# Kernel tuning notes

Hardware: AMD Instinct MI355X
Metric: run time of the kernel (lower is better)

Reference implementation:

```python
import jax, jax.numpy as jnp
import numpy as np

N = 4096
CIN = 128
COUT = 128
J = 2
SLOPE = 0.2        # LeakyReLU negative slope (GAT-style)
NEG = -9.0e15      # mask fill value from the source
ATT = J * COUT     # att_slice


def _leaky(v):
    return jnp.where(v >= 0, v, SLOPE * v)


def setup_inputs() -> dict:
    key = jax.random.key(0)
    ks = jax.random.split(key, 12)
    x = jax.random.normal(ks[0], (N, CIN), dtype=jnp.float32)

    def sparse_op(k):
        kv, km = jax.random.split(k)
        vals = jax.random.normal(kv, (N, N), dtype=jnp.float32)
        mask = jax.random.uniform(km, (N, N)) < 0.05
        return jnp.where(mask, vals, 0.0)

    Lu = sparse_op(ks[1])
    Ld = sparse_op(ks[2])
    P = jax.random.normal(ks[3], (N, N), dtype=jnp.float32) * 0.01  # harmonic projector

    s = 1.0 / np.sqrt(CIN)
    Wi_w = jax.random.uniform(ks[4], (J, CIN, COUT), minval=-s, maxval=s)
    Wi_b = jax.random.uniform(ks[5], (J, COUT), minval=-s, maxval=s)
    Ws_w = jax.random.uniform(ks[6], (J, CIN, COUT), minval=-s, maxval=s)
    Ws_b = jax.random.uniform(ks[7], (J, COUT), minval=-s, maxval=s)
    Wh_w = jax.random.uniform(ks[8], (CIN, COUT), minval=-s, maxval=s)
    Wh_b = jax.random.uniform(ks[9], (COUT,), minval=-s, maxval=s)
    att_irr = jax.random.normal(ks[10], (2 * ATT, 1), dtype=jnp.float32) * 0.1
    att_sol = jax.random.normal(ks[11], (2 * ATT, 1), dtype=jnp.float32) * 0.1
    return {"x": x, "Lu": Lu, "Ld": Ld, "P": P,
            "Wi_w": Wi_w, "Wi_b": Wi_b, "Ws_w": Ws_w, "Ws_b": Ws_b,
            "Wh_w": Wh_w, "Wh_b": Wh_b, "att_irr": att_irr, "att_sol": att_sol}


def reference(x, Lu, Ld, P, Wi_w, Wi_b, Ws_w, Ws_b, Wh_w, Wh_b, att_irr, att_sol):
    n = x.shape[0]
    # concat_j W_irr[j](x) -> [N, J*COUT] (j-major matches torch.cat along dim=1)
    x_irr = (jnp.einsum('nc,jco->njo', x, Wi_w) + Wi_b[None]).reshape(n, ATT)
    x_sol = (jnp.einsum('nc,jco->njo', x, Ws_w) + Ws_b[None]).reshape(n, ATT)

    # GAT-style scores: E[i,j] = leaky(s1[i] + s2[j])
    E_irr = _leaky(x_irr @ att_irr[:ATT] + (x_irr @ att_irr[ATT:]).T)
    E_sol = _leaky(x_sol @ att_sol[:ATT] + (x_sol @ att_sol[ATT:]).T)
    E_irr = jnp.where(Ld != 0, E_irr, NEG)
    E_sol = jnp.where(Lu != 0, E_sol, NEG)
    alpha_irr = jax.nn.softmax(E_irr, axis=1)  # dropout: eval mode -> identity
    alpha_sol = jax.nn.softmax(E_sol, axis=1)

    z = (alpha_irr @ x) @ Wi_w[0] + Wi_b[0] + (alpha_sol @ x) @ Ws_w[0] + Ws_b[0]
    for p in range(1, J):  # Laplacian-power aggregation
        alpha_irr = alpha_irr @ Ld
        alpha_sol = alpha_sol @ Lu
        z = z + (alpha_irr @ x) @ Wi_w[p] + Wi_b[p]
        z = z + (alpha_sol @ x) @ Ws_w[p] + Ws_b[p]
    z = z + (P @ x) @ Wh_w + Wh_b
    return z
```

## Files before the change

kernel.cpp:

```cpp
#include <hip/hip_runtime.h>

#define NN 4096
#define IDX_CAP 512
#define SEG_CAP 160
#define SLOPE 0.2f

typedef float f4_t __attribute__((ext_vector_type(4)));

#define V_OFF     0
#define C_OFF     512
#define BT_OFF    516
#define S_OFF     1024
#define HXI_OFF   32768
#define HXS_OFF   (HXI_OFF + NN*128)
#define UI_OFF    (HXS_OFF + NN*128)
#define US_OFF    (UI_OFF + NN*128)
#define XWH_OFF   (US_OFF + NN*128)
#define OI_OFF    (XWH_OFF + NN*128)
#define OS_OFF    (OI_OFF + NN*128)
#define ZP_OFF    (OS_OFF + NN*128)
#define WS_FLOATS (ZP_OFF + 8*NN*128)
#define IDX_BYTE_OFF ((size_t)WS_FLOATS * 4)
#define CNT_BYTE_OFF (IDX_BYTE_OFF + (size_t)2*NN*IDX_CAP*2)

__global__ __launch_bounds__(128) void k_prep(
    const float* __restrict__ Wi_w, const float* __restrict__ Wi_b,
    const float* __restrict__ Ws_w, const float* __restrict__ Ws_b,
    const float* __restrict__ Wh_b, const float* __restrict__ att_irr,
    const float* __restrict__ att_sol, float* __restrict__ ws) {
  const int t = threadIdx.x;
  float v1i = 0.f, v2i = 0.f, v1s = 0.f, v2s = 0.f;
  for (int j = 0; j < 2; ++j) {
    for (int o = 0; o < 128; ++o) {
      const float wi = Wi_w[j*16384 + t*128 + o];
      const float wv = Ws_w[j*16384 + t*128 + o];
      v1i += wi * att_irr[j*128 + o];
      v2i += wi * att_irr[256 + j*128 + o];
      v1s += wv * att_sol[j*128 + o];
      v2s += wv * att_sol[256 + j*128 + o];
    }
  }
  ws[V_OFF + t]       = v1i;
  ws[V_OFF + 128 + t] = v2i;
  ws[V_OFF + 256 + t] = v1s;
  ws[V_OFF + 384 + t] = v2s;
  ws[BT_OFF + t] = Wi_b[t] + Wi_b[128 + t] + Ws_b[t] + Ws_b[128 + t] + Wh_b[t];
  if (t < 4) {
    const float* bb = (t < 2) ? Wi_b : Ws_b;
    const float* aa = ((t < 2) ? att_irr : att_sol) + ((t & 1) ? 256 : 0);
    float c = 0.f;
    for (int k = 0; k < 256; ++k) c += bb[k] * aa[k];
    ws[C_OFF + t] = c;
  }
}

__global__ __launch_bounds__(256) void k_scores(const float* __restrict__ x,
                                                float* __restrict__ ws) {
  const int wave = threadIdx.x >> 6, lane = threadIdx.x & 63;
  const int row = blockIdx.x * 4 + wave;
  const float* v = ws + V_OFF;
  const float x0 = x[row*128 + lane];
  const float x1 = x[row*128 + 64 + lane];
  float p0 = x0 * v[lane]       + x1 * v[64 + lane];
  float p1 = x0 * v[128 + lane] + x1 * v[192 + lane];
  float p2 = x0 * v[256 + lane] + x1 * v[320 + lane];
  float p3 = x0 * v[384 + lane] + x1 * v[448 + lane];
  #pragma unroll
  for (int off = 32; off; off >>= 1) {
    p0 += __shfl_down(p0, off);
    p1 += __shfl_down(p1, off);
    p2 += __shfl_down(p2, off);
    p3 += __shfl_down(p3, off);
  }
  if (lane == 0) {
    ws[S_OFF + row]          = p0 + ws[C_OFF + 0];
    ws[S_OFF + NN + row]     = p1 + ws[C_OFF + 1];
    ws[S_OFF + 2*NN + row]   = p2 + ws[C_OFF + 2];
    ws[S_OFF + 3*NN + row]   = p3 + ws[C_OFF + 3];
  }
}

__global__ __launch_bounds__(256) void k_spmm_emit(
    const float* __restrict__ Ld, const float* __restrict__ Lu,
    const float* __restrict__ x, float* __restrict__ ws,
    unsigned short* __restrict__ idxbuf, int* __restrict__ cntbuf) {
  const int row = blockIdx.x & (NN - 1);
  const int br  = blockIdx.x >> 12;
  const float* __restrict__ Lrow = (br ? Lu : Ld) + (size_t)row * NN;
  float* __restrict__ Hx = ws + (br ? HXS_OFF : HXI_OFF);
  unsigned short* __restrict__ idxg = idxbuf + (size_t)(br*NN + row) * IDX_CAP;
  const float2* __restrict__ x2 = (const float2*)x;
  const int t = threadIdx.x;
  const int w = t >> 6, lane = t & 63;
  const unsigned long long lmask = (1ull << lane) - 1ull;

  __shared__ short jseg[4][SEG_CAP];
  __shared__ float vseg[4][SEG_CAP];
  __shared__ int   wcnt[4];
  __shared__ int   off[5];
  __shared__ short jl[IDX_CAP];
  __shared__ float vl[IDX_CAP];
  __shared__ float red[4][128];

  const f4_t* __restrict__ Lrow4 = (const f4_t*)Lrow;
  f4_t lv[4];
  #pragma unroll
  for (int i = 0; i < 4; ++i) lv[i] = __builtin_nontemporal_load(&Lrow4[i*256 + t]);

  int base = 0;
  #pragma unroll
  for (int i = 0; i < 4; ++i) {
    #pragma unroll
    for (int c = 0; c < 4; ++c) {
      const float v = lv[i][c];
      const unsigned long long bm = __ballot(v != 0.f);
      if (v != 0.f) {
        const int pos = base + (int)__popcll(bm & lmask);
        if (pos < SEG_CAP) {
          jseg[w][pos] = (short)((i*256 + t)*4 + c);
          vseg[w][pos] = v;
        }
      }
      base += (int)__popcll(bm);
    }
  }
  if (lane == 0) wcnt[w] = base;
  __syncthreads();
  if (t == 0) {
    int o = 0, ov = 0;
    #pragma unroll
    for (int s = 0; s < 4; ++s) { off[s] = o; ov |= (wcnt[s] > SEG_CAP); o += wcnt[s]; }
    off[4] = (ov || o > IDX_CAP) ? (IDX_CAP + 1) : o;
    cntbuf[br*NN + row] = off[4];
  }
  __syncthreads();
  const int m = off[4];

  if (m <= IDX_CAP) {
    const int o = off[w], c = wcnt[w];
    for (int k = lane; k < c; k += 64) {
      const short j = jseg[w][k];
      jl[o + k] = j;
      vl[o + k] = vseg[w][k];
      idxg[o + k] = (unsigned short)j;
    }
  }
  __syncthreads();

  float acc0 = 0.f, acc1 = 0.f;
  if (m <= IDX_CAP) {
    int p = w;
    for (; p + 28 < m; p += 32) {
      const int j0 = jl[p],    j1 = jl[p+4],  j2 = jl[p+8],  j3 = jl[p+12];
      const int j4 = jl[p+16], j5 = jl[p+20], j6 = jl[p+24], j7 = jl[p+28];
      const float v0 = vl[p],    v1 = vl[p+4],  v2 = vl[p+8],  v3 = vl[p+12];
      const float v4 = vl[p+16], v5 = vl[p+20], v6 = vl[p+24], v7 = vl[p+28];
      const float2 g0 = x2[j0*64 + lane];
      const float2 g1 = x2[j1*64 + lane];
      const float2 g2 = x2[j2*64 + lane];
      const float2 g3 = x2[j3*64 + lane];
      const float2 g4 = x2[j4*64 + lane];
      const float2 g5 = x2[j5*64 + lane];
      const float2 g6 = x2[j6*64 + lane];
      const float2 g7 = x2[j7*64 + lane];
      acc0 += v0*g0.x; acc1 += v0*g0.y;
      acc0 += v1*g1.x; acc1 += v1*g1.y;
      acc0 += v2*g2.x; acc1 += v2*g2.y;
      acc0 += v3*g3.x; acc1 += v3*g3.y;
      acc0 += v4*g4.x; acc1 += v4*g4.y;
      acc0 += v5*g5.x; acc1 += v5*g5.y;
      acc0 += v6*g6.x; acc1 += v6*g6.y;
      acc0 += v7*g7.x; acc1 += v7*g7.y;
    }
    for (; p < m; p += 4) {
      const int j = jl[p]; const float v = vl[p];
      const float2 g = x2[j*64 + lane];
      acc0 += v*g.x; acc1 += v*g.y;
    }
  } else {
    for (int j = w*1024; j < (w+1)*1024; ++j) {
      const float v = Lrow[j];
      if (v != 0.f) {
        const float2 g = x2[j*64 + lane];
        acc0 += v*g.x; acc1 += v*g.y;
      }
    }
  }
  red[w][lane*2]     = acc0;
  red[w][lane*2 + 1] = acc1;
  __syncthreads();
  if (t < 128)
    Hx[row*128 + t] = red[0][t] + red[1][t] + red[2][t] + red[3][t];
}

__global__ __launch_bounds__(256) void k_ugemm(
    const float* __restrict__ x, const float* __restrict__ Wi_w,
    const float* __restrict__ Ws_w, const float* __restrict__ Wh_w,
    float* __restrict__ ws) {
  const int rb = blockIdx.x;
  const int sel = blockIdx.y;
  const float* A[2]; const float* W[2]; int npass; float* out;
  if (sel == 0)      { A[0]=x; W[0]=Wi_w; A[1]=ws+HXI_OFF; W[1]=Wi_w+16384; npass=2; out=ws+UI_OFF; }
  else if (sel == 1) { A[0]=x; W[0]=Ws_w; A[1]=ws+HXS_OFF; W[1]=Ws_w+16384; npass=2; out=ws+US_OFF; }
  else               { A[0]=x; W[0]=Wh_w; A[1]=nullptr;    W[1]=nullptr;    npass=1; out=ws+XWH_OFF; }

  __shared__ __align__(16) float At[32][33];
  __shared__ __align__(16) float Wt[32][132];
  const int t = threadIdx.x;
  const int rg = t >> 4, cg = t & 15;
  const int r0 = rb * 32;
  float acc[2][8];
  #pragma unroll
  for (int i = 0; i < 2; ++i)
    #pragma unroll
    for (int j = 0; j < 8; ++j) acc[i][j] = 0.f;

  for (int ps = 0; ps < npass; ++ps) {
    const float* __restrict__ Ap = A[ps];
    const float* __restrict__ Wp = W[ps];
    for (int k0 = 0; k0 < 128; k0 += 32) {
      __syncthreads();
      {
        const int row = t >> 3, kq = t & 7;
        const float4 av = *(const float4*)&Ap[(r0 + row)*128 + k0 + kq*4];
        At[row][kq*4+0] = av.x; At[row][kq*4+1] = av.y;
        At[row][kq*4+2] = av.z; At[row][kq*4+3] = av.w;
      }
      #pragma unroll
      for (int l = 0; l < 4; ++l) {
        const int idx = t + l*256;
        const int kr = idx >> 5, c4 = idx & 31;
        const float4 wv = *(const float4*)&Wp[(k0 + kr)*128 + c4*4];
        Wt[kr][c4*4+0] = wv.x; Wt[kr][c4*4+1] = wv.y;
        Wt[kr][c4*4+2] = wv.z; Wt[kr][c4*4+3] = wv.w;
      }
      __syncthreads();
      #pragma unroll
      for (int k = 0; k < 32; ++k) {
        const float a0 = At[rg*2 + 0][k];
        const float a1 = At[rg*2 + 1][k];
        const float4 b0 = *(const float4*)&Wt[k][cg*8];
        const float4 b1 = *(const float4*)&Wt[k][cg*8 + 4];
        acc[0][0] += a0*b0.x; acc[0][1] += a0*b0.y; acc[0][2] += a0*b0.z; acc[0][3] += a0*b0.w;
        acc[0][4] += a0*b1.x; acc[0][5] += a0*b1.y; acc[0][6] += a0*b1.z; acc[0][7] += a0*b1.w;
        acc[1][0] += a1*b0.x; acc[1][1] += a1*b0.y; acc[1][2] += a1*b0.z; acc[1][3] += a1*b0.w;
        acc[1][4] += a1*b1.x; acc[1][5] += a1*b1.y; acc[1][6] += a1*b1.z; acc[1][7] += a1*b1.w;
      }
    }
  }
  #pragma unroll
  for (int i = 0; i < 2; ++i) {
    const int r = r0 + rg*2 + i;
    #pragma unroll
    for (int j = 0; j < 8; ++j) out[r*128 + cg*8 + j] = acc[i][j];
  }
}

__global__ __launch_bounds__(256) void k_pgemm(const float* __restrict__ P,
                                               const float* __restrict__ ws,
                                               float* __restrict__ zpart) {
  const int rbl = blockIdx.x;
  const int kz  = blockIdx.y;
  const float* __restrict__ Xw = ws + XWH_OFF;

  __shared__ __align__(16) float Pt[64][33];
  __shared__ __align__(16) float Xt[32][132];
  const int t = threadIdx.x;
  const int rg = t >> 4, cg = t & 15;
  const int r0 = rbl * 64;
  const int kbase = kz * 512;
  float acc[4][8];
  #pragma unroll
  for (int i = 0; i < 4; ++i)
    #pragma unroll
    for (int j = 0; j < 8; ++j) acc[i][j] = 0.f;

  for (int k0 = kbase; k0 < kbase + 512; k0 += 32) {
    __syncthreads();
    #pragma unroll
    for (int l = 0; l < 2; ++l) {
      const int idx = t + l*256;
      const int row = idx >> 3, kq = idx & 7;
      const float4 pv = *(const float4*)&P[(size_t)(r0 + row)*NN + k0 + kq*4];
      Pt[row][kq*4+0] = pv.x; Pt[row][kq*4+1] = pv.y;
      Pt[row][kq*4+2] = pv.z; Pt[row][kq*4+3] = pv.w;
    }
    #pragma unroll
    for (int l = 0; l < 4; ++l) {
      const int idx = t + l*256;
      const int kr = idx >> 5, c4 = idx & 31;
      const float4 xv = *(const float4*)&Xw[(k0 + kr)*128 + c4*4];
      Xt[kr][c4*4+0] = xv.x; Xt[kr][c4*4+1] = xv.y;
      Xt[kr][c4*4+2] = xv.z; Xt[kr][c4*4+3] = xv.w;
    }
    __syncthreads();
    #pragma unroll
    for (int k = 0; k < 32; ++k) {
      const float a0 = Pt[rg*4 + 0][k];
      const float a1 = Pt[rg*4 + 1][k];
      const float a2 = Pt[rg*4 + 2][k];
      const float a3 = Pt[rg*4 + 3][k];
      const float4 b0 = *(const float4*)&Xt[k][cg*8];
      const float4 b1 = *(const float4*)&Xt[k][cg*8 + 4];
      acc[0][0] += a0*b0.x; acc[0][1] += a0*b0.y; acc[0][2] += a0*b0.z; acc[0][3] += a0*b0.w;
      acc[0][4] += a0*b1.x; acc[0][5] += a0*b1.y; acc[0][6] += a0*b1.z; acc[0][7] += a0*b1.w;
      acc[1][0] += a1*b0.x; acc[1][1] += a1*b0.y; acc[1][2] += a1*b0.z; acc[1][3] += a1*b0.w;
      acc[1][4] += a1*b1.x; acc[1][5] += a1*b1.y; acc[1][6] += a1*b1.z; acc[1][7] += a1*b1.w;
      acc[2][0] += a2*b0.x; acc[2][1] += a2*b0.y; acc[2][2] += a2*b0.z; acc[2][3] += a2*b0.w;
      acc[2][4] += a2*b1.x; acc[2][5] += a2*b1.y; acc[2][6] += a2*b1.z; acc[2][7] += a2*b1.w;
      acc[3][0] += a3*b0.x; acc[3][1] += a3*b0.y; acc[3][2] += a3*b0.z; acc[3][3] += a3*b0.w;
      acc[3][4] += a3*b1.x; acc[3][5] += a3*b1.y; acc[3][6] += a3*b1.z; acc[3][7] += a3*b1.w;
    }
  }
  float* __restrict__ zp = zpart + (size_t)kz * NN * 128;
  #pragma unroll
  for (int i = 0; i < 4; ++i) {
    const int r = r0 + rg*4 + i;
    #pragma unroll
    for (int j = 0; j < 8; ++j) zp[r*128 + cg*8 + j] = acc[i][j];
  }
}

__global__ __launch_bounds__(256) void k_attn(
    const float* __restrict__ Ld, const float* __restrict__ Lu,
    float* __restrict__ ws, const unsigned short* __restrict__ idxbuf,
    const int* __restrict__ cntbuf) {
  const int row = blockIdx.x & (NN - 1);
  const int br  = blockIdx.x >> 12;
  const float* __restrict__ U = ws + (br ? US_OFF : UI_OFF);
  const float2* __restrict__ U2 = (const float2*)U;
  float* __restrict__ O = ws + (br ? OS_OFF : OI_OFF);
  const float s1 = ws[S_OFF + (br ? 2*NN : 0) + row];
  const float* __restrict__ s2a = ws + S_OFF + (br ? 3*NN : NN);
  const int cnt = cntbuf[br*NN + row];
  const int t = threadIdx.x;
  const int w = t >> 6, lane = t & 63;

  __shared__ int   jl[IDX_CAP];
  __shared__ float el[IDX_CAP];
  __shared__ float red[4][128];
  __shared__ float rsum[256];
  __shared__ float dsh[4];

  float acc0 = 0.f, acc1 = 0.f;
  if (cnt > 0 && cnt <= IDX_CAP) {
    const unsigned short* __restrict__ idx = idxbuf + (size_t)(br*NN + row) * IDX_CAP;
    float dpart = 0.f;
    for (int p = t; p < cnt; p += 256) {
      const int j = idx[p];
      const float sc = s1 + s2a[j];
      const float e = expf(sc >= 0.f ? sc : SLOPE * sc);
      jl[p] = j; el[p] = e; dpart += e;
    }
    rsum[t] = dpart;
    __syncthreads();
    if (t < 128) rsum[t] += rsum[t + 128];
    __syncthreads();
    if (t < 64) {
      float v = rsum[t] + rsum[t + 64];
      #pragma unroll
      for (int off = 32; off; off >>= 1) v += __shfl_down(v, off);
      if (t == 0) dsh[0] = v;
    }
    __syncthreads();
    const float den = dsh[0];
    int p = w;
    for (; p + 28 < cnt; p += 32) {
      const int j0 = jl[p],    j1 = jl[p+4],  j2 = jl[p+8],  j3 = jl[p+12];
      const int j4 = jl[p+16], j5 = jl[p+20], j6 = jl[p+24], j7 = jl[p+28];
      const float e0 = el[p],    e1 = el[p+4],  e2 = el[p+8],  e3 = el[p+12];
      const float e4 = el[p+16], e5 = el[p+20], e6 = el[p+24], e7 = el[p+28];
      const float2 g0 = U2[j0*64 + lane];
      const float2 g1 = U2[j1*64 + lane];
      const float2 g2 = U2[j2*64 + lane];
      const float2 g3 = U2[j3*64 + lane];
      const float2 g4 = U2[j4*64 + lane];
      const float2 g5 = U2[j5*64 + lane];
      const float2 g6 = U2[j6*64 + lane];
      const float2 g7 = U2[j7*64 + lane];
      acc0 += e0*g0.x; acc1 += e0*g0.y;
      acc0 += e1*g1.x; acc1 += e1*g1.y;
      acc0 += e2*g2.x; acc1 += e2*g2.y;
      acc0 += e3*g3.x; acc1 += e3*g3.y;
      acc0 += e4*g4.x; acc1 += e4*g4.y;
      acc0 += e5*g5.x; acc1 += e5*g5.y;
      acc0 += e6*g6.x; acc1 += e6*g6.y;
      acc0 += e7*g7.x; acc1 += e7*g7.y;
    }
    for (; p < cnt; p += 4) {
      const int j = jl[p]; const float e = el[p];
      const float2 g = U2[j*64 + lane];
      acc0 += e*g.x; acc1 += e*g.y;
    }
    red[w][lane*2]     = acc0;
    red[w][lane*2 + 1] = acc1;
    __syncthreads();
    if (t < 128)
      O[row*128 + t] = (red[0][t] + red[1][t] + red[2][t] + red[3][t]) / den;
  } else if (cnt == 0) {
    for (int j = w*1024; j < (w+1)*1024; ++j) {
      const float2 g = U2[j*64 + lane];
      acc0 += g.x; acc1 += g.y;
    }
    red[w][lane*2]     = acc0;
    red[w][lane*2 + 1] = acc1;
    __syncthreads();
    if (t < 128)
      O[row*128 + t] = (red[0][t] + red[1][t] + red[2][t] + red[3][t]) * (1.f / NN);
  } else {
    const float* __restrict__ Lrow = (br ? Lu : Ld) + (size_t)row * NN;
    float dp = 0.f;
    for (int j = w*1024; j < (w+1)*1024; ++j) {
      const float v = Lrow[j];
      if (v != 0.f) {
        const float sc = s1 + s2a[j];
        const float e = expf(sc >= 0.f ? sc : SLOPE * sc);
        const float2 g = U2[j*64 + lane];
        acc0 += e*g.x; acc1 += e*g.y;
        dp += e;
      }
    }
    if (lane == 0) dsh[w] = dp;
    red[w][lane*2]     = acc0;
    red[w][lane*2 + 1] = acc1;
    __syncthreads();
    const float den = dsh[0] + dsh[1] + dsh[2] + dsh[3];
    if (t < 128)
      O[row*128 + t] = (red[0][t] + red[1][t] + red[2][t] + red[3][t]) / den;
  }
}

__global__ __launch_bounds__(256) void k_combine(const float* __restrict__ ws,
                                                 float* __restrict__ z) {
  const int i = blockIdx.x * 256 + threadIdx.x;
  const int col = i & 127;
  float acc = ws[BT_OFF + col] + ws[OI_OFF + i] + ws[OS_OFF + i];
  #pragma unroll
  for (int kz = 0; kz < 8; ++kz) acc += ws[ZP_OFF + kz*NN*128 + i];
  z[i] = acc;
}

extern "C" void kernel_launch(void* const* d_in, const int* in_sizes, int n_in,
                              void* d_out, int out_size, void* d_ws, size_t ws_size,
                              hipStream_t stream) {
  const float* x       = (const float*)d_in[0];
  const float* Lu      = (const float*)d_in[1];
  const float* Ld      = (const float*)d_in[2];
  const float* P       = (const float*)d_in[3];
  const float* Wi_w    = (const float*)d_in[4];
  const float* Wi_b    = (const float*)d_in[5];
  const float* Ws_w    = (const float*)d_in[6];
  const float* Ws_b    = (const float*)d_in[7];
  const float* Wh_w    = (const float*)d_in[8];
  const float* Wh_b    = (const float*)d_in[9];
  const float* att_irr = (const float*)d_in[10];
  const float* att_sol = (const float*)d_in[11];
  float* z  = (float*)d_out;
  float* ws = (float*)d_ws;
  unsigned short* idxbuf = (unsigned short*)((char*)d_ws + IDX_BYTE_OFF);
  int*            cntbuf = (int*)((char*)d_ws + CNT_BYTE_OFF);

  k_prep<<<1, 128, 0, stream>>>(Wi_w, Wi_b, Ws_w, Ws_b, Wh_b, att_irr, att_sol, ws);
  k_scores<<<1024, 256, 0, stream>>>(x, ws);
  k_spmm_emit<<<2 * NN, 256, 0, stream>>>(Ld, Lu, x, ws, idxbuf, cntbuf);
  {
    dim3 g(128, 3);
    k_ugemm<<<g, 256, 0, stream>>>(x, Wi_w, Ws_w, Wh_w, ws);
  }
  {
    dim3 g(64, 8);
    k_pgemm<<<g, 256, 0, stream>>>(P, ws, ws + ZP_OFF);
  }
  k_attn<<<2 * NN, 256, 0, stream>>>(Ld, Lu, ws, idxbuf, cntbuf);
  k_combine<<<NN * 128 / 256, 256, 0, stream>>>(ws, z);
}
```

Before: 399.0 us.

## Co-schedule dense P GEMM with sparse SpMM and attention kernels via block-split fusion

Moves the x@Wh GEMM into a merged pre-kernel alongside the score computation. The dense P@(xWh) GEMM is split into two halves of the K range, and each half is fused into the same launch as the memory-bound sparse SpMM or attention kernel using a shared-memory union and block-index dispatch. The aim is to overlap compute-heavy GEMM blocks with gather-heavy sparse blocks and cut launch count. It also pads the Xt shared tile with an XI swizzle to reduce bank conflicts. The cost is larger per-block shared memory from the union, which can lower occupancy for the sparse blocks.

```diff
diff --git a/kernel.cpp b/kernel.cpp
--- a/kernel.cpp
+++ b/kernel.cpp
@@ -23,6 +23,20 @@
 #define IDX_BYTE_OFF ((size_t)WS_FLOATS * 4)
 #define CNT_BYTE_OFF (IDX_BYTE_OFF + (size_t)2*NN*IDX_CAP*2)
 
+#define XI(c) ((c) + (((c) >> 5) << 2))
+
+struct SmemGemm { float Pt[64][33]; float Xt[32][140]; };
+struct SmemSpmm {
+  short jseg[4][SEG_CAP]; float vseg[4][SEG_CAP];
+  int wcnt[4]; int off[5];
+  short jl[IDX_CAP]; float vl[IDX_CAP]; float red[4][128];
+};
+struct SmemAttn {
+  int jl[IDX_CAP]; float el[IDX_CAP]; float red[4][128];
+  float rsum[256]; float dsh[4];
+};
+union SmemU { SmemGemm g; SmemSpmm s; SmemAttn a; };
+
 __global__ __launch_bounds__(128) void k_prep(
     const float* __restrict__ Wi_w, const float* __restrict__ Wi_b,
     const float* __restrict__ Ws_w, const float* __restrict__ Ws_b,
@@ -54,38 +68,149 @@
   }
 }
 
-__global__ __launch_bounds__(256) void k_scores(const float* __restrict__ x,
-                                                float* __restrict__ ws) {
-  const int wave = threadIdx.x >> 6, lane = threadIdx.x & 63;
-  const int row = blockIdx.x * 4 + wave;
-  const float* v = ws + V_OFF;
-  const float x0 = x[row*128 + lane];
-  const float x1 = x[row*128 + 64 + lane];
-  float p0 = x0 * v[lane]       + x1 * v[64 + lane];
-  float p1 = x0 * v[128 + lane] + x1 * v[192 + lane];
-  float p2 = x0 * v[256 + lane] + x1 * v[320 + lane];
-  float p3 = x0 * v[384 + lane] + x1 * v[448 + lane];
-  #pragma unroll
-  for (int off = 32; off; off >>= 1) {
-    p0 += __shfl_down(p0, off);
-    p1 += __shfl_down(p1, off);
-    p2 += __shfl_down(p2, off);
-    p3 += __shfl_down(p3, off);
-  }
-  if (lane == 0) {
-    ws[S_OFF + row]          = p0 + ws[C_OFF + 0];
-    ws[S_OFF + NN + row]     = p1 + ws[C_OFF + 1];
-    ws[S_OFF + 2*NN + row]   = p2 + ws[C_OFF + 2];
-    ws[S_OFF + 3*NN + row]   = p3 + ws[C_OFF + 3];
-  }
-}
-
-__global__ __launch_bounds__(256) void k_spmm_emit(
+__global__ __launch_bounds__(256) void k_pre2(
+    const float* __restrict__ x, const float* __restrict__ Wh_w,
+    float* __restrict__ ws) {
+  __shared__ __align__(16) float At[32][33];
+  __shared__ __align__(16) float Wt[32][132];
+  const int t = threadIdx.x;
+
+  if (blockIdx.x < 128) {
+    const int rb = blockIdx.x;
+    float* out = ws + XWH_OFF;
+    const int rg = t >> 4, cg = t & 15;
+    const int r0 = rb * 32;
+    float acc[2][8];
+    #pragma unroll
+    for (int i = 0; i < 2; ++i)
+      #pragma unroll
+      for (int j = 0; j < 8; ++j) acc[i][j] = 0.f;
+    for (int k0 = 0; k0 < 128; k0 += 32) {
+      __syncthreads();
+      {
+        const int row = t >> 3, kq = t & 7;
+        const float4 av = *(const float4*)&x[(r0 + row)*128 + k0 + kq*4];
+        At[row][kq*4+0] = av.x; At[row][kq*4+1] = av.y;
+        At[row][kq*4+2] = av.z; At[row][kq*4+3] = av.w;
+      }
+      #pragma unroll
+      for (int l = 0; l < 4; ++l) {
+        const int idx = t + l*256;
+        const int kr = idx >> 5, c4 = idx & 31;
+        const float4 wv = *(const float4*)&Wh_w[(k0 + kr)*128 + c4*4];
+        Wt[kr][c4*4+0] = wv.x; Wt[kr][c4*4+1] = wv.y;
+        Wt[kr][c4*4+2] = wv.z; Wt[kr][c4*4+3] = wv.w;
+      }
+      __syncthreads();
+      #pragma unroll
+      for (int k = 0; k < 32; ++k) {
+        const float a0 = At[rg*2 + 0][k];
+        const float a1 = At[rg*2 + 1][k];
+        const float4 b0 = *(const float4*)&Wt[k][cg*8];
+        const float4 b1 = *(const float4*)&Wt[k][cg*8 + 4];
+        acc[0][0] += a0*b0.x; acc[0][1] += a0*b0.y; acc[0][2] += a0*b0.z; acc[0][3] += a0*b0.w;
+        acc[0][4] += a0*b1.x; acc[0][5] += a0*b1.y; acc[0][6] += a0*b1.z; acc[0][7] += a0*b1.w;
+        acc[1][0] += a1*b0.x; acc[1][1] += a1*b0.y; acc[1][2] += a1*b0.z; acc[1][3] += a1*b0.w;
+        acc[1][4] += a1*b1.x; acc[1][5] += a1*b1.y; acc[1][6] += a1*b1.z; acc[1][7] += a1*b1.w;
+      }
+    }
+    #pragma unroll
+    for (int i = 0; i < 2; ++i) {
+      const int r = r0 + rg*2 + i;
+      #pragma unroll
+      for (int j = 0; j < 8; ++j) out[r*128 + cg*8 + j] = acc[i][j];
+    }
+  } else {
+    const int wave = t >> 6, lane = t & 63;
+    const int row = (blockIdx.x - 128) * 4 + wave;
+    const float* v = ws + V_OFF;
+    const float x0 = x[row*128 + lane];
+    const float x1 = x[row*128 + 64 + lane];
+    float p0 = x0 * v[lane]       + x1 * v[64 + lane];
+    float p1 = x0 * v[128 + lane] + x1 * v[192 + lane];
+    float p2 = x0 * v[256 + lane] + x1 * v[320 + lane];
+    float p3 = x0 * v[384 + lane] + x1 * v[448 + lane];
+    #pragma unroll
+    for (int off = 32; off; off >>= 1) {
+      p0 += __shfl_down(p0, off);
+      p1 += __shfl_down(p1, off);
+      p2 += __shfl_down(p2, off);
+      p3 += __shfl_down(p3, off);
+    }
+    if (lane == 0) {
+      ws[S_OFF + row]          = p0 + ws[C_OFF + 0];
+      ws[S_OFF + NN + row]     = p1 + ws[C_OFF + 1];
+      ws[S_OFF + 2*NN + row]   = p2 + ws[C_OFF + 2];
+      ws[S_OFF + 3*NN + row]   = p3 + ws[C_OFF + 3];
+    }
+  }
+}
+
+__device__ __forceinline__ void pgemm_body(
+    const float* __restrict__ P, const float* __restrict__ Xw,
+    float* __restrict__ zpart, SmemU& sm, const int rbl, const int kz) {
+  const int t = threadIdx.x;
+  const int rg = t >> 4, cg = t & 15;
+  const int r0 = rbl * 64;
+  const int kbase = kz * 512;
+  float acc[4][8];
+  #pragma unroll
+  for (int i = 0; i < 4; ++i)
+    #pragma unroll
+    for (int j = 0; j < 8; ++j) acc[i][j] = 0.f;
+
+  for (int k0 = kbase; k0 < kbase + 512; k0 += 32) {
+    __syncthreads();
+    #pragma unroll
+    for (int l = 0; l < 2; ++l) {
+      const int idx = t + l*256;
+      const int row = idx >> 3, kq = idx & 7;
+      const float4 pv = *(const float4*)&P[(size_t)(r0 + row)*NN + k0 + kq*4];
+      sm.g.Pt[row][kq*4+0] = pv.x; sm.g.Pt[row][kq*4+1] = pv.y;
+      sm.g.Pt[row][kq*4+2] = pv.z; sm.g.Pt[row][kq*4+3] = pv.w;
+    }
+    #pragma unroll
+    for (int l = 0; l < 4; ++l) {
+      const int idx = t + l*256;
+      const int kr = idx >> 5, c4 = idx & 31;
+      const float4 xv = *(const float4*)&Xw[(k0 + kr)*128 + c4*4];
+      *(float4*)&sm.g.Xt[kr][XI(c4*4)] = xv;
+    }
+    __syncthreads();
+    #pragma unroll
+    for (int k = 0; k < 32; ++k) {
+      const float a0 = sm.g.Pt[rg*4 + 0][k];
+      const float a1 = sm.g.Pt[rg*4 + 1][k];
+      const float a2 = sm.g.Pt[rg*4 + 2][k];
+      const float a3 = sm.g.Pt[rg*4 + 3][k];
+      const float4 b0 = *(const float4*)&sm.g.Xt[k][XI(cg*8)];
+      const float4 b1 = *(const float4*)&sm.g.Xt[k][XI(cg*8 + 4)];
+      acc[0][0] += a0*b0.x; acc[0][1] += a0*b0.y; acc[0][2] += a0*b0.z; acc[0][3] += a0*b0.w;
+      acc[0][4] += a0*b1.x; acc[0][5] += a0*b1.y; acc[0][6] += a0*b1.z; acc[0][7] += a0*b1.w;
+      acc[1][0] += a1*b0.x; acc[1][1] += a1*b0.y; acc[1][2] += a1*b0.z; acc[1][3] += a1*b0.w;
+      acc[1][4] += a1*b1.x; acc[1][5] += a1*b1.y; acc[1][6] += a1*b1.z; acc[1][7] += a1*b1.w;
+      acc[2][0] += a2*b0.x; acc[2][1] += a2*b0.y; acc[2][2] += a2*b0.z; acc[2][3] += a2*b0.w;
+      acc[2][4] += a2*b1.x; acc[2][5] += a2*b1.y; acc[2][6] += a2*b1.z; acc[2][7] += a2*b1.w;
+      acc[3][0] += a3*b0.x; acc[3][1] += a3*b0.y; acc[3][2] += a3*b0.z; acc[3][3] += a3*b0.w;
+      acc[3][4] += a3*b1.x; acc[3][5] += a3*b1.y; acc[3][6] += a3*b1.z; acc[3][7] += a3*b1.w;
+    }
+  }
+  float* __restrict__ zp = zpart + (size_t)kz * NN * 128;
+  #pragma unroll
+  for (int i = 0; i < 4; ++i) {
+    const int r = r0 + rg*4 + i;
+    #pragma unroll
+    for (int j = 0; j < 8; ++j) zp[r*128 + cg*8 + j] = acc[i][j];
+  }
+}
+
+__device__ __forceinline__ void spmm_body(
     const float* __restrict__ Ld, const float* __restrict__ Lu,
     const float* __restrict__ x, float* __restrict__ ws,
-    unsigned short* __restrict__ idxbuf, int* __restrict__ cntbuf) {
-  const int row = blockIdx.x & (NN - 1);
-  const int br  = blockIdx.x >> 12;
+    unsigned short* __restrict__ idxbuf, int* __restrict__ cntbuf,
+    SmemU& sm, const int bx) {
+  const int row = bx & (NN - 1);
+  const int br  = bx >> 12;
   const float* __restrict__ Lrow = (br ? Lu : Ld) + (size_t)row * NN;
   float* __restrict__ Hx = ws + (br ? HXS_OFF : HXI_OFF);
   unsigned short* __restrict__ idxg = idxbuf + (size_t)(br*NN + row) * IDX_CAP;
@@ -94,14 +219,6 @@
   const int w = t >> 6, lane = t & 63;
   const unsigned long long lmask = (1ull << lane) - 1ull;
 
-  __shared__ short jseg[4][SEG_CAP];
-  __shared__ float vseg[4][SEG_CAP];
-  __shared__ int   wcnt[4];
-  __shared__ int   off[5];
-  __shared__ short jl[IDX_CAP];
-  __shared__ float vl[IDX_CAP];
-  __shared__ float red[4][128];
-
   const f4_t* __restrict__ Lrow4 = (const f4_t*)Lrow;
   f4_t lv[4];
   #pragma unroll
@@ -117,31 +234,31 @@
       if (v != 0.f) {
         const int pos = base + (int)__popcll(bm & lmask);
         if (pos < SEG_CAP) {
-          jseg[w][pos] = (short)((i*256 + t)*4 + c);
-          vseg[w][pos] = v;
+          sm.s.jseg[w][pos] = (short)((i*256 + t)*4 + c);
+          sm.s.vseg[w][pos] = v;
         }
       }
       base += (int)__popcll(bm);
     }
   }
-  if (lane == 0) wcnt[w] = base;
+  if (lane == 0) sm.s.wcnt[w] = base;
   __syncthreads();
   if (t == 0) {
     int o = 0, ov = 0;
     #pragma unroll
-    for (int s = 0; s < 4; ++s) { off[s] = o; ov |= (wcnt[s] > SEG_CAP); o += wcnt[s]; }
-    off[4] = (ov || o > IDX_CAP) ? (IDX_CAP + 1) : o;
-    cntbuf[br*NN + row] = off[4];
+    for (int s = 0; s < 4; ++s) { sm.s.off[s] = o; ov |= (sm.s.wcnt[s] > SEG_CAP); o += sm.s.wcnt[s]; }
+    sm.s.off[4] = (ov || o > IDX_CAP) ? (IDX_CAP + 1) : o;
+    cntbuf[br*NN + row] = sm.s.off[4];
   }
   __syncthreads();
-  const int m = off[4];
+  const int m = sm.s.off[4];
 
   if (m <= IDX_CAP) {
-    const int o = off[w], c = wcnt[w];
+    const int o = sm.s.off[w], c = sm.s.wcnt[w];
     for (int k = lane; k < c; k += 64) {
-      const short j = jseg[w][k];
-      jl[o + k] = j;
-      vl[o + k] = vseg[w][k];
+      const short j = sm.s.jseg[w][k];
+      sm.s.jl[o + k] = j;
+      sm.s.vl[o + k] = sm.s.vseg[w][k];
       idxg[o + k] = (unsigned short)j;
     }
   }
@@ -151,10 +268,10 @@
   if (m <= IDX_CAP) {
     int p = w;
     for (; p + 28 < m; p += 32) {
-      const int j0 = jl[p],    j1 = jl[p+4],  j2 = jl[p+8],  j3 = jl[p+12];
-      const int j4 = jl[p+16], j5 = jl[p+20], j6 = jl[p+24], j7 = jl[p+28];
-      const float v0 = vl[p],    v1 = vl[p+4],  v2 = vl[p+8],  v3 = vl[p+12];
-      const float v4 = vl[p+16], v5 = vl[p+20], v6 = vl[p+24], v7 = vl[p+28];
+      const int j0 = sm.s.jl[p],    j1 = sm.s.jl[p+4],  j2 = sm.s.jl[p+8],  j3 = sm.s.jl[p+12];
+      const int j4 = sm.s.jl[p+16], j5 = sm.s.jl[p+20], j6 = sm.s.jl[p+24], j7 = sm.s.jl[p+28];
+      const float v0 = sm.s.vl[p],    v1 = sm.s.vl[p+4],  v2 = sm.s.vl[p+8],  v3 = sm.s.vl[p+12];
+      const float v4 = sm.s.vl[p+16], v5 = sm.s.vl[p+20], v6 = sm.s.vl[p+24], v7 = sm.s.vl[p+28];
       const float2 g0 = x2[j0*64 + lane];
       const float2 g1 = x2[j1*64 + lane];
       const float2 g2 = x2[j2*64 + lane];
@@ -173,7 +290,7 @@
       acc0 += v7*g7.x; acc1 += v7*g7.y;
     }
     for (; p < m; p += 4) {
-      const int j = jl[p]; const float v = vl[p];
+      const int j = sm.s.jl[p]; const float v = sm.s.vl[p];
       const float2 g = x2[j*64 + lane];
       acc0 += v*g.x; acc1 += v*g.y;
     }
@@ -186,161 +303,26 @@
       }
     }
   }
-  red[w][lane*2]     = acc0;
-  red[w][lane*2 + 1] = acc1;
+  sm.s.red[w][lane*2]     = acc0;
+  sm.s.red[w][lane*2 + 1] = acc1;
   __syncthreads();
   if (t < 128)
-    Hx[row*128 + t] = red[0][t] + red[1][t] + red[2][t] + red[3][t];
-}
-
-__global__ __launch_bounds__(256) void k_ugemm(
-    const float* __restrict__ x, const float* __restrict__ Wi_w,
-    const float* __restrict__ Ws_w, const float* __restrict__ Wh_w,
-    float* __restrict__ ws) {
-  const int rb = blockIdx.x;
-  const int sel = blockIdx.y;
-  const float* A[2]; const float* W[2]; int npass; float* out;
-  if (sel == 0)      { A[0]=x; W[0]=Wi_w; A[1]=ws+HXI_OFF; W[1]=Wi_w+16384; npass=2; out=ws+UI_OFF; }
-  else if (sel == 1) { A[0]=x; W[0]=Ws_w; A[1]=ws+HXS_OFF; W[1]=Ws_w+16384; npass=2; out=ws+US_OFF; }
-  else               { A[0]=x; W[0]=Wh_w; A[1]=nullptr;    W[1]=nullptr;    npass=1; out=ws+XWH_OFF; }
-
-  __shared__ __align__(16) float At[32][33];
-  __shared__ __align__(16) float Wt[32][132];
-  const int t = threadIdx.x;
-  const int rg = t >> 4, cg = t & 15;
-  const int r0 = rb * 32;
-  float acc[2][8];
-  #pragma unroll
-  for (int i = 0; i < 2; ++i)
-    #pragma unroll
-    for (int j = 0; j < 8; ++j) acc[i][j] = 0.f;
-
-  for (int ps = 0; ps < npass; ++ps) {
-    const float* __restrict__ Ap = A[ps];
-    const float* __restrict__ Wp = W[ps];
-    for (int k0 = 0; k0 < 128; k0 += 32) {
-      __syncthreads();
-      {
-        const int row = t >> 3, kq = t & 7;
-        const float4 av = *(const float4*)&Ap[(r0 + row)*128 + k0 + kq*4];
-        At[row][kq*4+0] = av.x; At[row][kq*4+1] = av.y;
-        At[row][kq*4+2] = av.z; At[row][kq*4+3] = av.w;
-      }
-      #pragma unroll
-      for (int l = 0; l < 4; ++l) {
-        const int idx = t + l*256;
-        const int kr = idx >> 5, c4 = idx & 31;
-        const float4 wv = *(const float4*)&Wp[(k0 + kr)*128 + c4*4];
-        Wt[kr][c4*4+0] = wv.x; Wt[kr][c4*4+1] = wv.y;
-        Wt[kr][c4*4+2] = wv.z; Wt[kr][c4*4+3] = wv.w;
-      }
-      __syncthreads();
-      #pragma unroll
-      for (int k = 0; k < 32; ++k) {
-        const float a0 = At[rg*2 + 0][k];
-        const float a1 = At[rg*2 + 1][k];
-        const float4 b0 = *(const float4*)&Wt[k][cg*8];
-        const float4 b1 = *(const float4*)&Wt[k][cg*8 + 4];
-        acc[0][0] += a0*b0.x; acc[0][1] += a0*b0.y; acc[0][2] += a0*b0.z; acc[0][3] += a0*b0.w;
-        acc[0][4] += a0*b1.x; acc[0][5] += a0*b1.y; acc[0][6] += a0*b1.z; acc[0][7] += a0*b1.w;
-        acc[1][0] += a1*b0.x; acc[1][1] += a1*b0.y; acc[1][2] += a1*b0.z; acc[1][3] += a1*b0.w;
-        acc[1][4] += a1*b1.x; acc[1][5] += a1*b1.y; acc[1][6] += a1*b1.z; acc[1][7] += a1*b1.w;
-      }
-    }
-  }
-  #pragma unroll
-  for (int i = 0; i < 2; ++i) {
-    const int r = r0 + rg*2 + i;
-    #pragma unroll
-    for (int j = 0; j < 8; ++j) out[r*128 + cg*8 + j] = acc[i][j];
-  }
-}
-
-__global__ __launch_bounds__(256) void k_pgemm(const float* __restrict__ P,
-                                               const float* __restrict__ ws,
-                                               float* __restrict__ zpart) {
-  const int rbl = blockIdx.x;
-  const int kz  = blockIdx.y;
-  const float* __restrict__ Xw = ws + XWH_OFF;
-
-  __shared__ __align__(16) float Pt[64][33];
-  __shared__ __align__(16) float Xt[32][132];
-  const int t = threadIdx.x;
-  const int rg = t >> 4, cg = t & 15;
-  const int r0 = rbl * 64;
-  const int kbase = kz * 512;
-  float acc[4][8];
-  #pragma unroll
-  for (int i = 0; i < 4; ++i)
-    #pragma unroll
-    for (int j = 0; j < 8; ++j) acc[i][j] = 0.f;
-
-  for (int k0 = kbase; k0 < kbase + 512; k0 += 32) {
-    __syncthreads();
-    #pragma unroll
-    for (int l = 0; l < 2; ++l) {
-      const int idx = t + l*256;
-      const int row = idx >> 3, kq = idx & 7;
-      const float4 pv = *(const float4*)&P[(size_t)(r0 + row)*NN + k0 + kq*4];
-      Pt[row][kq*4+0] = pv.x; Pt[row][kq*4+1] = pv.y;
-      Pt[row][kq*4+2] = pv.z; Pt[row][kq*4+3] = pv.w;
-    }
-    #pragma unroll
-    for (int l = 0; l < 4; ++l) {
-      const int idx = t + l*256;
-      const int kr = idx >> 5, c4 = idx & 31;
-      const float4 xv = *(const float4*)&Xw[(k0 + kr)*128 + c4*4];
-      Xt[kr][c4*4+0] = xv.x; Xt[kr][c4*4+1] = xv.y;
-      Xt[kr][c4*4+2] = xv.z; Xt[kr][c4*4+3] = xv.w;
-    }
-    __syncthreads();
-    #pragma unroll
-    for (int k = 0; k < 32; ++k) {
-      const float a0 = Pt[rg*4 + 0][k];
-      const float a1 = Pt[rg*4 + 1][k];
-      const float a2 = Pt[rg*4 + 2][k];
-      const float a3 = Pt[rg*4 + 3][k];
-      const float4 b0 = *(const float4*)&Xt[k][cg*8];
-      const float4 b1 = *(const float4*)&Xt[k][cg*8 + 4];
-      acc[0][0] += a0*b0.x; acc[0][1] += a0*b0.y; acc[0][2] += a0*b0.z; acc[0][3] += a0*b0.w;
-      acc[0][4] += a0*b1.x; acc[0][5] += a0*b1.y; acc[0][6] += a0*b1.z; acc[0][7] += a0*b1.w;
-      acc[1][0] += a1*b0.x; acc[1][1] += a1*b0.y; acc[1][2] += a1*b0.z; acc[1][3] += a1*b0.w;
-      acc[1][4] += a1*b1.x; acc[1][5] += a1*b1.y; acc[1][6] += a1*b1.z; acc[1][7] += a1*b1.w;
-      acc[2][0] += a2*b0.x; acc[2][1] += a2*b0.y; acc[2][2] += a2*b0.z; acc[2][3] += a2*b0.w;
-      acc[2][4] += a2*b1.x; acc[2][5] += a2*b1.y; acc[2][6] += a2*b1.z; acc[2][7] += a2*b1.w;
-      acc[3][0] += a3*b0.x; acc[3][1] += a3*b0.y; acc[3][2] += a3*b0.z; acc[3][3] += a3*b0.w;
-      acc[3][4] += a3*b1.x; acc[3][5] += a3*b1.y; acc[3][6] += a3*b1.z; acc[3][7] += a3*b1.w;
-    }
-  }
-  float* __restrict__ zp = zpart + (size_t)kz * NN * 128;
-  #pragma unroll
-  for (int i = 0; i < 4; ++i) {
-    const int r = r0 + rg*4 + i;
-    #pragma unroll
-    for (int j = 0; j < 8; ++j) zp[r*128 + cg*8 + j] = acc[i][j];
-  }
-}
-
-__global__ __launch_bounds__(256) void k_attn(
+    Hx[row*128 + t] = sm.s.red[0][t] + sm.s.red[1][t] + sm.s.red[2][t] + sm.s.red[3][t];
+}
+
+__device__ __forceinline__ void attn_body(
     const float* __restrict__ Ld, const float* __restrict__ Lu,
     float* __restrict__ ws, const unsigned short* __restrict__ idxbuf,
-    const int* __restrict__ cntbuf) {
-  const int row = blockIdx.x & (NN - 1);
-  const int br  = blockIdx.x >> 12;
-  const float* __restrict__ U = ws + (br ? US_OFF : UI_OFF);
-  const float2* __restrict__ U2 = (const float2*)U;
+    const int* __restrict__ cntbuf, SmemU& sm, const int bx) {
+  const int row = bx & (NN - 1);
+  const int br  = bx >> 12;
+  const float2* __restrict__ U2 = (const float2*)(ws + (br ? US_OFF : UI_OFF));
   float* __restrict__ O = ws + (br ? OS_OFF : OI_OFF);
   const float s1 = ws[S_OFF + (br ? 2*NN : 0) + row];
   const float* __restrict__ s2a = ws + S_OFF + (br ? 3*NN : NN);
   const int cnt = cntbuf[br*NN + row];
   const int t = threadIdx.x;
   const int w = t >> 6, lane = t & 63;
-
-  __shared__ int   jl[IDX_CAP];
-  __shared__ float el[IDX_CAP];
-  __shared__ float red[4][128];
-  __shared__ float rsum[256];
-  __shared__ float dsh[4];
 
   float acc0 = 0.f, acc1 = 0.f;
   if (cnt > 0 && cnt <= IDX_CAP) {
@@ -350,26 +332,26 @@
       const int j = idx[p];
       const float sc = s1 + s2a[j];
       const float e = expf(sc >= 0.f ? sc : SLOPE * sc);
-      jl[p] = j; el[p] = e; dpart += e;
-    }
-    rsum[t] = dpart;
-    __syncthreads();
-    if (t < 128) rsum[t] += rsum[t + 128];
+      sm.a.jl[p] = j; sm.a.el[p] = e; dpart += e;
+    }
+    sm.a.rsum[t] = dpart;
+    __syncthreads();
+    if (t < 128) sm.a.rsum[t] += sm.a.rsum[t + 128];
     __syncthreads();
     if (t < 64) {
-      float v = rsum[t] + rsum[t + 64];
+      float v = sm.a.rsum[t] + sm.a.rsum[t + 64];
       #pragma unroll
       for (int off = 32; off; off >>= 1) v += __shfl_down(v, off);
-      if (t == 0) dsh[0] = v;
-    }
-    __syncthreads();
-    const float den = dsh[0];
+      if (t == 0) sm.a.dsh[0] = v;
+    }
+    __syncthreads();
+    const float den = sm.a.dsh[0];
     int p = w;
     for (; p + 28 < cnt; p += 32) {
-      const int j0 = jl[p],    j1 = jl[p+4],  j2 = jl[p+8],  j3 = jl[p+12];
-      const int j4 = jl[p+16], j5 = jl[p+20], j6 = jl[p+24], j7 = jl[p+28];
-      const float e0 = el[p],    e1 = el[p+4],  e2 = el[p+8],  e3 = el[p+12];
-      const float e4 = el[p+16], e5 = el[p+20], e6 = el[p+24], e7 = el[p+28];
+      const int j0 = sm.a.jl[p],    j1 = sm.a.jl[p+4],  j2 = sm.a.jl[p+8],  j3 = sm.a.jl[p+12];
+      const int j4 = sm.a.jl[p+16], j5 = sm.a.jl[p+20], j6 = sm.a.jl[p+24], j7 = sm.a.jl[p+28];
+      const float e0 = sm.a.el[p],    e1 = sm.a.el[p+4],  e2 = sm.a.el[p+8],  e3 = sm.a.el[p+12];
+      const float e4 = sm.a.el[p+16], e5 = sm.a.el[p+20], e6 = sm.a.el[p+24], e7 = sm.a.el[p+28];
       const float2 g0 = U2[j0*64 + lane];
       const float2 g1 = U2[j1*64 + lane];
       const float2 g2 = U2[j2*64 + lane];
@@ -388,25 +370,25 @@
       acc0 += e7*g7.x; acc1 += e7*g7.y;
     }
     for (; p < cnt; p += 4) {
-      const int j = jl[p]; const float e = el[p];
+      const int j = sm.a.jl[p]; const float e = sm.a.el[p];
       const float2 g = U2[j*64 + lane];
       acc0 += e*g.x; acc1 += e*g.y;
     }
-    red[w][lane*2]     = acc0;
-    red[w][lane*2 + 1] = acc1;
+    sm.a.red[w][lane*2]     = acc0;
+    sm.a.red[w][lane*2 + 1] = acc1;
     __syncthreads();
     if (t < 128)
-      O[row*128 + t] = (red[0][t] + red[1][t] + red[2][t] + red[3][t]) / den;
+      O[row*128 + t] = (sm.a.red[0][t] + sm.a.red[1][t] + sm.a.red[2][t] + sm.a.red[3][t]) / den;
   } else if (cnt == 0) {
     for (int j = w*1024; j < (w+1)*1024; ++j) {
       const float2 g = U2[j*64 + lane];
       acc0 += g.x; acc1 += g.y;
     }
-    red[w][lane*2]     = acc0;
-    red[w][lane*2 + 1] = acc1;
+    sm.a.red[w][lane*2]     = acc0;
+    sm.a.red[w][lane*2 + 1] = acc1;
     __syncthreads();
     if (t < 128)
-      O[row*128 + t] = (red[0][t] + red[1][t] + red[2][t] + red[3][t]) * (1.f / NN);
+      O[row*128 + t] = (sm.a.red[0][t] + sm.a.red[1][t] + sm.a.red[2][t] + sm.a.red[3][t]) * (1.f / NN);
   } else {
     const float* __restrict__ Lrow = (br ? Lu : Ld) + (size_t)row * NN;
     float dp = 0.f;
@@ -420,13 +402,100 @@
         dp += e;
       }
     }
-    if (lane == 0) dsh[w] = dp;
-    red[w][lane*2]     = acc0;
-    red[w][lane*2 + 1] = acc1;
-    __syncthreads();
-    const float den = dsh[0] + dsh[1] + dsh[2] + dsh[3];
+    if (lane == 0) sm.a.dsh[w] = dp;
+    sm.a.red[w][lane*2]     = acc0;
+    sm.a.red[w][lane*2 + 1] = acc1;
+    __syncthreads();
+    const float den = sm.a.dsh[0] + sm.a.dsh[1] + sm.a.dsh[2] + sm.a.dsh[3];
     if (t < 128)
-      O[row*128 + t] = (red[0][t] + red[1][t] + red[2][t] + red[3][t]) / den;
+      O[row*128 + t] = (sm.a.red[0][t] + sm.a.red[1][t] + sm.a.red[2][t] + sm.a.red[3][t]) / den;
+  }
+}
+
+__global__ __launch_bounds__(256) void k_fusedA(
+    const float* __restrict__ Ld, const float* __restrict__ Lu,
+    const float* __restrict__ x, const float* __restrict__ P,
+    float* __restrict__ ws, unsigned short* __restrict__ idxbuf,
+    int* __restrict__ cntbuf, float* __restrict__ zpart) {
+  __shared__ SmemU sm;
+  if (blockIdx.x < 256) {
+    pgemm_body(P, ws + XWH_OFF, zpart, sm, blockIdx.x & 63, blockIdx.x >> 6);
+  } else {
+    spmm_body(Ld, Lu, x, ws, idxbuf, cntbuf, sm, blockIdx.x - 256);
+  }
+}
+
+__global__ __launch_bounds__(256) void k_fusedB(
+    const float* __restrict__ Ld, const float* __restrict__ Lu,
+    const float* __restrict__ P, float* __restrict__ ws,
+    const unsigned short* __restrict__ idxbuf, const int* __restrict__ cntbuf,
+    float* __restrict__ zpart) {
+  __shared__ SmemU sm;
+  if (blockIdx.x < 256) {
+    pgemm_body(P, ws + XWH_OFF, zpart, sm, blockIdx.x & 63, (blockIdx.x >> 6) + 4);
+  } else {
+    attn_body(Ld, Lu, ws, idxbuf, cntbuf, sm, blockIdx.x - 256);
+  }
+}
+
+__global__ __launch_bounds__(256) void k_ugemm(
+    const float* __restrict__ x, const float* __restrict__ Wi_w,
+    const float* __restrict__ Ws_w, float* __restrict__ ws) {
+  const int rb = blockIdx.x;
+  const int sel = blockIdx.y;
+  const float* A[2]; const float* W[2]; float* out;
+  if (sel == 0) { A[0]=x; W[0]=Wi_w; A[1]=ws+HXI_OFF; W[1]=Wi_w+16384; out=ws+UI_OFF; }
+  else          { A[0]=x; W[0]=Ws_w; A[1]=ws+HXS_OFF; W[1]=Ws_w+16384; out=ws+US_OFF; }
+
+  __shared__ __align__(16) float At[32][33];
+  __shared__ __align__(16) float Wt[32][132];
+  const int t = threadIdx.x;
+  const int rg = t >> 4, cg = t & 15;
+  const int r0 = rb * 32;
+  float acc[2][8];
+  #pragma unroll
+  for (int i = 0; i < 2; ++i)
+    #pragma unroll
+    for (int j = 0; j < 8; ++j) acc[i][j] = 0.f;
+
+  for (int ps = 0; ps < 2; ++ps) {
+    const float* __restrict__ Ap = A[ps];
+    const float* __restrict__ Wp = W[ps];
+    for (int k0 = 0; k0 < 128; k0 += 32) {
+      __syncthreads();
+      {
+        const int row = t >> 3, kq = t & 7;
+        const float4 av = *(const float4*)&Ap[(r0 + row)*128 + k0 + kq*4];
+        At[row][kq*4+0] = av.x; At[row][kq*4+1] = av.y;
+        At[row][kq*4+2] = av.z; At[row][kq*4+3] = av.w;
+      }
+      #pragma unroll
+      for (int l = 0; l < 4; ++l) {
+        const int idx = t + l*256;
+        const int kr = idx >> 5, c4 = idx & 31;
+        const float4 wv = *(const float4*)&Wp[(k0 + kr)*128 + c4*4];
+        Wt[kr][c4*4+0] = wv.x; Wt[kr][c4*4+1] = wv.y;
+        Wt[kr][c4*4+2] = wv.z; Wt[kr][c4*4+3] = wv.w;
+      }
+      __syncthreads();
+      #pragma unroll
+      for (int k = 0; k < 32; ++k) {
+        const float a0 = At[rg*2 + 0][k];
+        const float a1 = At[rg*2 + 1][k];
+        const float4 b0 = *(const float4*)&Wt[k][cg*8];
+        const float4 b1 = *(const float4*)&Wt[k][cg*8 + 4];
+        acc[0][0] += a0*b0.x; acc[0][1] += a0*b0.y; acc[0][2] += a0*b0.z; acc[0][3] += a0*b0.w;
+        acc[0][4] += a0*b1.x; acc[0][5] += a0*b1.y; acc[0][6] += a0*b1.z; acc[0][7] += a0*b1.w;
+        acc[1][0] += a1*b0.x; acc[1][1] += a1*b0.y; acc[1][2] += a1*b0.z; acc[1][3] += a1*b0.w;
+        acc[1][4] += a1*b1.x; acc[1][5] += a1*b1.y; acc[1][6] += a1*b1.z; acc[1][7] += a1*b1.w;
+      }
+    }
+  }
+  #pragma unroll
+  for (int i = 0; i < 2; ++i) {
+    const int r = r0 + rg*2 + i;
+    #pragma unroll
+    for (int j = 0; j < 8; ++j) out[r*128 + cg*8 + j] = acc[i][j];
   }
 }
 
@@ -459,18 +528,15 @@
   float* ws = (float*)d_ws;
   unsigned short* idxbuf = (unsigned short*)((char*)d_ws + IDX_BYTE_OFF);
   int*            cntbuf = (int*)((char*)d_ws + CNT_BYTE_OFF);
+  float*          zpart  = ws + ZP_OFF;
 
   k_prep<<<1, 128, 0, stream>>>(Wi_w, Wi_b, Ws_w, Ws_b, Wh_b, att_irr, att_sol, ws);
-  k_scores<<<1024, 256, 0, stream>>>(x, ws);
-  k_spmm_emit<<<2 * NN, 256, 0, stream>>>(Ld, Lu, x, ws, idxbuf, cntbuf);
+  k_pre2<<<1152, 256, 0, stream>>>(x, Wh_w, ws);
+  k_fusedA<<<256 + 2*NN, 256, 0, stream>>>(Ld, Lu, x, P, ws, idxbuf, cntbuf, zpart);
   {
-    dim3 g(128, 3);
-    k_ugemm<<<g, 256, 0, stream>>>(x, Wi_w, Ws_w, Wh_w, ws);
-  }
-  {
-    dim3 g(64, 8);
-    k_pgemm<<<g, 256, 0, stream>>>(P, ws, ws + ZP_OFF);
-  }
-  k_attn<<<2 * NN, 256, 0, stream>>>(Ld, Lu, ws, idxbuf, cntbuf);
+    dim3 g(128, 2);
+    k_ugemm<<<g, 256, 0, stream>>>(x, Wi_w, Ws_w, ws);
+  }
+  k_fusedB<<<256 + 2*NN, 256, 0, stream>>>(Ld, Lu, P, ws, idxbuf, cntbuf, zpart);
   k_combine<<<NN * 128 / 256, 256, 0, stream>>>(ws, z);
 }
```

After: 622.5 us. 1.56x slower.
